# Optimization experiments

Hardware: AMD Instinct MI355X
Metric: run time of the kernel (lower is better)

Reference implementation:

```python
import jax, jax.numpy as jnp
import numpy as np

TEMP = 0.7
ALPHA_ADV = 1.0
BETA_BAND = 0.5
BAND_L = 0.05
BAND_H = 0.2
W_HEUR = 0.5
W_LEAR = 0.5


def setup_inputs() -> dict:
    key = jax.random.key(0)
    ks = jax.random.split(key, 6)
    B, Sn, C, H, W = 2, 5, 64, 192, 192
    hid = 64
    return {
        "S": jax.random.normal(ks[0], (B, C, H, W), jnp.float32),
        "T": jax.random.normal(ks[1], (B, Sn, C, H, W), jnp.float32),
        "adapt_w": jax.random.normal(ks[2], (Sn, C, C), jnp.float32) / np.sqrt(C).astype(np.float32),
        "adapt_b": jnp.zeros((Sn, C), jnp.float32),
        "r_w1": jax.random.normal(ks[3], (hid, Sn * C * 3), jnp.float32) * 0.05,
        "r_b1": jnp.zeros((hid,), jnp.float32),
        "r_w2": jax.random.normal(ks[4], (Sn, hid), jnp.float32) * 0.05,
        "r_b2": jnp.zeros((Sn,), jnp.float32),
        "ema_mu": jnp.zeros((1, Sn, C, 1, 1), jnp.float32),
        "ema_sigma": jnp.ones((1, Sn, C, 1, 1), jnp.float32),
        "ema_proxy": jnp.zeros((1, Sn, 1, 1, 1), jnp.float32),
    }


def reference(S, T, adapt_w, adapt_b, r_w1, r_b1, r_w2, r_b2, ema_mu, ema_sigma, ema_proxy):
    B, Sn, C, H, W = T.shape
    bias = adapt_b[None, :, :, None, None]
    # per-sweep 1x1 conv == per-sweep channel matmul
    T_adapt = jnp.einsum('sdc,bschw->bsdhw', adapt_w, T) + bias          # [B,S,C,H,W]
    S_rep = jnp.einsum('sdc,bchw->bsdhw', adapt_w, S) + bias             # [B,S,C,H,W]
    Tz = (T_adapt - ema_mu) / ema_sigma
    Sz = (S_rep - ema_mu) / ema_sigma
    delta = Tz - Sz
    proxy = jnp.mean(delta * delta, axis=2, keepdims=True)               # [B,S,1,H,W]
    cur = jnp.mean(proxy, axis=(0, 3, 4), keepdims=True)                 # [1,S,1,1,1]
    # heuristic score (gamma_ucb = 0 -> no UCB term)
    impr = jax.lax.stop_gradient(ema_proxy - cur)
    adv = impr - jnp.mean(impr, axis=1, keepdims=True)
    below = jnp.maximum(BAND_L - cur, 0.0)
    above = jnp.maximum(cur - BAND_H, 0.0)
    band = -(below * below + above * above)
    score = ALPHA_ADV * adv + BETA_BAND * band                           # [1,S,1,1,1]
    score_heur = jnp.broadcast_to(score, proxy.shape)[:, :, 0]           # [B,S,H,W]
    # learned router: concat along channel of each sweep then 1x1 MLP
    x = jnp.concatenate([Sz, Tz, delta], axis=2).reshape(B, Sn * 3 * C, H, W)
    h = jax.nn.relu(jnp.einsum('oi,bihw->bohw', r_w1, x) + r_b1[None, :, None, None])
    score_learn = jnp.einsum('oi,bihw->bohw', r_w2, h) + r_b2[None, :, None, None]
    logits = W_HEUR * score_heur + W_LEAR * score_learn                  # [B,S,H,W]
    weights = jax.nn.softmax(logits / TEMP, axis=1)                      # soft gating over sweeps
    return weights
```

## Files before the change

kernel.cpp:

```cpp
#include <hip/hip_runtime.h>
#include <math.h>

#define HWSZ 36864
#define NWID 2304

typedef short bf16x8 __attribute__((ext_vector_type(8)));
typedef float f32x16 __attribute__((ext_vector_type(16)));
typedef unsigned int u32x4 __attribute__((ext_vector_type(4)));

__device__ __forceinline__ unsigned short f2bf(float x) {
    unsigned u = __float_as_uint(x);
    return (unsigned short)((u + 0x7fffu + ((u >> 16) & 1u)) >> 16);
}

__device__ __forceinline__ void block_sync_lds() {
    __builtin_amdgcn_sched_barrier(0);
    asm volatile("s_waitcnt lgkmcnt(0)" ::: "memory");
    __builtin_amdgcn_s_barrier();
    __builtin_amdgcn_sched_barrier(0);
}

__global__ void pre_all(const float* __restrict__ rw1, const float* __restrict__ rb1,
                        const float* __restrict__ aw, const float* __restrict__ ab,
                        const float* __restrict__ mu, const float* __restrict__ sg,
                        unsigned short* __restrict__ AfragW,
                        unsigned short* __restrict__ AfragMS2, float* __restrict__ c1) {
    int i = blockIdx.x * 256 + threadIdx.x;
    if (i < 40960) {
        int s = i / 8192, rem = i % 8192;
        int r = rem / 2048, rem2 = rem % 2048;
        int t = rem2 / 512, q = rem2 % 512;
        int l = q >> 3, e = q & 7;
        int R = 32 * r + (l & 31);
        int k = 16 * t + 8 * (l >> 5) + e;
        float v;
        if (R < 64) {
            v = aw[s * 4096 + R * 64 + k] / sg[s * 64 + R];
        } else {
            int o = R - 64;
            const float* wp = rw1 + o * 960 + s * 192;
            const float* A  = aw + s * 4096 + k;
            const float* G  = sg + s * 64;
            float sum = 0.f;
            #pragma unroll 8
            for (int d = 0; d < 64; ++d)
                sum = fmaf(wp[64 + d] + wp[128 + d], A[d * 64] / G[d], sum);
            v = sum;
        }
        AfragW[i] = f2bf(v);
    } else if (i < 45056) {
        int j = i - 40960;
        int r = j / 2048, rem2 = j % 2048;
        int t = rem2 / 512, q = rem2 % 512;
        int l = q >> 3, e = q & 7;
        int o = 32 * r + (l & 31);
        int k = 16 * t + 8 * (l >> 5) + e;
        float sum = 0.f;
        for (int s = 0; s < 5; ++s) {
            const float* wp = rw1 + o * 960 + s * 192;
            const float* A  = aw + s * 4096 + k;
            const float* G  = sg + s * 64;
            #pragma unroll 8
            for (int d = 0; d < 64; ++d)
                sum = fmaf(wp[d] - wp[128 + d], A[d * 64] / G[d], sum);
        }
        AfragMS2[j] = f2bf(sum);
    } else if (i < 45120) {
        int o = i - 45056;
        float sum = rb1[o];
        for (int s = 0; s < 5; ++s) {
            const float* wp = rw1 + o * 960 + s * 192;
            #pragma unroll 8
            for (int d = 0; d < 64; ++d) {
                int sd = s * 64 + d;
                sum = fmaf(wp[d] + wp[64 + d], (ab[sd] - mu[sd]) / sg[sd], sum);
            }
        }
        c1[o] = sum;
    }
}

__global__ __launch_bounds__(128, 4) void fused_main(
        const float* __restrict__ S, const float* __restrict__ T,
        const unsigned short* __restrict__ AfragW, const unsigned short* __restrict__ AfragMS2,
        const float* __restrict__ c1, const float* __restrict__ rw2, const float* __restrict__ rb2,
        float* __restrict__ slearn, float* __restrict__ partial) {
    __shared__ __align__(16) unsigned short sTile[2048];
    __shared__ __align__(16) unsigned short tbuf[2][2048];
    __shared__ float w2s[320];
    __shared__ float c1s[64];
    __shared__ float rb2s[8];
    __shared__ float wred[5][2];
    __shared__ float hpart[2][5][32];

    const int tid = threadIdx.x, lane = tid & 63, w = tid >> 6;
    const int hi = lane >> 5, pxm = lane & 31;
    const int blk = blockIdx.x;
    const int b = blk / 1152;
    const int pix0 = (blk % 1152) * 32;

    const int o8 = tid >> 4, pq = tid & 15;
    const float* Sp = S + ((size_t)(b * 64 + 8 * o8)) * HWSZ + pix0 + 2 * pq;
    const float* Tp = T + ((size_t)(b * 5 * 64 + 8 * o8)) * HWSZ + pix0 + 2 * pq;

    float2 RS[8], R[8];
    #pragma unroll
    for (int j = 0; j < 8; ++j) RS[j] = *(const float2*)(Sp + (size_t)j * HWSZ);
    #pragma unroll
    for (int j = 0; j < 8; ++j) R[j] = *(const float2*)(Tp + (size_t)j * HWSZ);

    for (int i = tid; i < 320; i += 128) w2s[i] = rw2[i];
    if (tid < 64) c1s[tid] = c1[tid];
    if (tid < 5)  rb2s[tid] = rb2[tid];

    auto slot = [](int px) { return px ^ (px >> 3); };

    auto packWrite = [&](unsigned short* dst, const float2* Rv) {
        #pragma unroll
        for (int pi = 0; pi < 2; ++pi) {
            int px = 2 * pq + pi;
            u32x4 v;
            #pragma unroll
            for (int jj = 0; jj < 4; ++jj) {
                float a = pi ? Rv[2 * jj].y : Rv[2 * jj].x;
                float c = pi ? Rv[2 * jj + 1].y : Rv[2 * jj + 1].x;
                v[jj] = (unsigned)f2bf(a) | ((unsigned)f2bf(c) << 16);
            }
            *(u32x4*)&dst[(o8 * 32 + slot(px)) * 8] = v;
        }
    };
    auto loadT = [&](float2* Rv, int s) {
        const float* p = Tp + (size_t)(s * 64) * HWSZ;
        #pragma unroll
        for (int j = 0; j < 8; ++j) Rv[j] = *(const float2*)(p + (size_t)j * HWSZ);
    };
    auto ldsB = [&](const unsigned short* buf, int kt) -> bf16x8 {
        return *(const bf16x8*)&buf[((kt * 2 + hi) * 32 + slot(pxm)) * 8];
    };

    const bf16x8* am = (const bf16x8*)AfragMS2 + lane;
    bf16x8 msf[4];
    #pragma unroll
    for (int kt = 0; kt < 4; ++kt) msf[kt] = am[(w * 4 + kt) * 64];

    packWrite(sTile, RS);
    block_sync_lds();

    bf16x8 bS[4];
    #pragma unroll
    for (int kt = 0; kt < 4; ++kt) bS[kt] = ldsB(sTile, kt);

    f32x16 hacc;
    #pragma unroll
    for (int i = 0; i < 16; ++i) hacc[i] = 0.f;
    #pragma unroll
    for (int kt = 0; kt < 4; ++kt)
        hacc = __builtin_amdgcn_mfma_f32_32x32x16_bf16(msf[kt], bS[kt], hacc, 0, 0, 0);

    packWrite(tbuf[0], R);
    loadT(R, 1);
    block_sync_lds();

    const bf16x8* afw = (const bf16x8*)AfragW + lane;

    #pragma unroll
    for (int s = 0; s < 5; ++s) {
        const unsigned short* cur = tbuf[s & 1];
        unsigned short* nxt = tbuf[(s + 1) & 1];

        bf16x8 fD[4], fM[4];
        #pragma unroll
        for (int kt = 0; kt < 4; ++kt) fD[kt] = afw[((s * 4 + w) * 4 + kt) * 64];
        #pragma unroll
        for (int kt = 0; kt < 4; ++kt) fM[kt] = afw[((s * 4 + 2 + w) * 4 + kt) * 64];

        if (s < 4) {
            packWrite(nxt, R);
            if (s < 3) loadT(R, s + 2);
        }

        f32x16 dacc;
        #pragma unroll
        for (int i = 0; i < 16; ++i) dacc[i] = 0.f;
        #pragma unroll
        for (int kt = 0; kt < 4; ++kt)
            dacc = __builtin_amdgcn_mfma_f32_32x32x16_bf16(fD[kt], bS[kt], dacc, 0, 0, 0);
        #pragma unroll
        for (int i = 0; i < 16; ++i) dacc[i] = -dacc[i];
        #pragma unroll
        for (int kt = 0; kt < 4; ++kt) {
            bf16x8 bT = ldsB(cur, kt);
            dacc = __builtin_amdgcn_mfma_f32_32x32x16_bf16(fD[kt], bT, dacc, 0, 0, 0);
            hacc = __builtin_amdgcn_mfma_f32_32x32x16_bf16(fM[kt], bT, hacc, 0, 0, 0);
        }

        float sq = 0.f;
        #pragma unroll
        for (int i = 0; i < 16; ++i) sq = fmaf(dacc[i], dacc[i], sq);
        #pragma unroll
        for (int m = 1; m < 64; m <<= 1) sq += __shfl_xor(sq, m, 64);
        if (lane == 0) wred[s][w] = sq;

        block_sync_lds();
    }

    #pragma unroll
    for (int i = 0; i < 16; ++i) {
        int row = (i & 3) + 8 * (i >> 2) + 4 * hi + 32 * w;
        hacc[i] = fmaxf(hacc[i] + c1s[row], 0.f);
    }
    #pragma unroll
    for (int sp = 0; sp < 5; ++sp) {
        float d = 0.f;
        #pragma unroll
        for (int i = 0; i < 16; ++i) {
            int row = (i & 3) + 8 * (i >> 2) + 4 * hi + 32 * w;
            d = fmaf(w2s[sp * 64 + row], hacc[i], d);
        }
        d += __shfl_xor(d, 32, 64);
        if (hi == 0) hpart[w][sp][pxm] = d;
    }
    block_sync_lds();
    if (tid < 5) partial[blk * 5 + tid] = wred[tid][0] + wred[tid][1];
    for (int i = tid; i < 160; i += 128) {
        int sp = i >> 5, px = i & 31;
        slearn[((size_t)(b * 5 + sp)) * HWSZ + pix0 + px] =
            hpart[0][sp][px] + hpart[1][sp][px] + rb2s[sp];
    }
}

__global__ void score_kernel(const float* __restrict__ partial,
                             const float* __restrict__ ema_proxy,
                             float* __restrict__ scoreBuf) {
    __shared__ float red[256];
    __shared__ float cur[5];
    int tid = threadIdx.x;
    for (int s = 0; s < 5; ++s) {
        float sum = 0.f;
        for (int i = tid; i < NWID; i += 256) sum += partial[i * 5 + s];
        red[tid] = sum;
        __syncthreads();
        for (int off = 128; off > 0; off >>= 1) {
            if (tid < off) red[tid] += red[tid + off];
            __syncthreads();
        }
        if (tid == 0) cur[s] = red[0] * (1.0f / (64.0f * 2.0f * HWSZ));
        __syncthreads();
    }
    if (tid == 0) {
        float impr[5]; float m = 0.f;
        for (int s = 0; s < 5; ++s) { impr[s] = ema_proxy[s] - cur[s]; m += impr[s]; }
        m *= 0.2f;
        for (int s = 0; s < 5; ++s) {
            float adv = impr[s] - m;
            float c = cur[s];
            float below = fmaxf(0.05f - c, 0.f);
            float above = fmaxf(c - 0.2f, 0.f);
            float band = -(below * below + above * above);
            scoreBuf[s] = 1.0f * adv + 0.5f * band;
        }
    }
}

__global__ void softmax_kernel(const float* __restrict__ slearn,
                               const float* __restrict__ scoreBuf,
                               float* __restrict__ out) {
    int i = blockIdx.x * 256 + threadIdx.x;
    if (i >= 2 * HWSZ) return;
    int b = i / HWSZ, p = i % HWSZ;
    float l[5];
    float mx = -1e30f;
    #pragma unroll
    for (int s = 0; s < 5; ++s) {
        float v = (0.5f * scoreBuf[s] + 0.5f * slearn[((size_t)(b * 5 + s)) * HWSZ + p]) / 0.7f;
        l[s] = v;
        mx = fmaxf(mx, v);
    }
    float sum = 0.f;
    #pragma unroll
    for (int s = 0; s < 5; ++s) { l[s] = expf(l[s] - mx); sum += l[s]; }
    float inv = 1.0f / sum;
    #pragma unroll
    for (int s = 0; s < 5; ++s) out[((size_t)(b * 5 + s)) * HWSZ + p] = l[s] * inv;
}

extern "C" void kernel_launch(void* const* d_in, const int* in_sizes, int n_in,
                              void* d_out, int out_size, void* d_ws, size_t ws_size,
                              hipStream_t stream) {
    const float* S   = (const float*)d_in[0];
    const float* T   = (const float*)d_in[1];
    const float* aw  = (const float*)d_in[2];
    const float* ab  = (const float*)d_in[3];
    const float* rw1 = (const float*)d_in[4];
    const float* rb1 = (const float*)d_in[5];
    const float* rw2 = (const float*)d_in[6];
    const float* rb2 = (const float*)d_in[7];
    const float* mu  = (const float*)d_in[8];
    const float* sg  = (const float*)d_in[9];
    const float* ep  = (const float*)d_in[10];

    float* ws = (float*)d_ws;
    float* c1f      = ws;
    float* scoreBuf = ws + 64;
    float* partial  = ws + 72;
    unsigned short* AfragW   = (unsigned short*)(ws + 11592);
    unsigned short* AfragMS2 = (unsigned short*)(ws + 32072);
    float* slearn   = ws + 34120;
    float* out = (float*)d_out;

    pre_all<<<177, 256, 0, stream>>>(rw1, rb1, aw, ab, mu, sg, AfragW, AfragMS2, c1f);
    fused_main<<<NWID, 128, 0, stream>>>(S, T, AfragW, AfragMS2, c1f, rw2, rb2, slearn, partial);
    score_kernel<<<1, 256, 0, stream>>>(partial, ep, scoreBuf);
    softmax_kernel<<<288, 256, 0, stream>>>(slearn, scoreBuf, out);
}
```

Baseline: 66.04 us.

## Process two 32-pixel tiles per block and double-buffer weight fragments

Each block now handles 64 pixels as two independent 32-pixel sub-tiles, so the grid is halved and the per-sweep weight fragments loaded from global memory are reused across both tiles. Weight fragments for the next sweep are prefetched into a second register set while the current sweep computes. Register and LDS use roughly doubles, so launch bounds drop to 2 blocks per SM-equivalent, trading occupancy for more loads in flight per wave and more MFMA work per fragment load.

```diff
diff --git a/kernel.cpp b/kernel.cpp
--- a/kernel.cpp
+++ b/kernel.cpp
@@ -3,6 +3,7 @@
 
 #define HWSZ 36864
 #define NWID 2304
+#define NBLK6 1152
 
 typedef short bf16x8 __attribute__((ext_vector_type(8)));
 typedef float f32x16 __attribute__((ext_vector_type(16)));
@@ -80,34 +81,40 @@
     }
 }
 
-__global__ __launch_bounds__(128, 4) void fused_main(
+__global__ __launch_bounds__(128, 2) void fused_main(
         const float* __restrict__ S, const float* __restrict__ T,
         const unsigned short* __restrict__ AfragW, const unsigned short* __restrict__ AfragMS2,
         const float* __restrict__ c1, const float* __restrict__ rw2, const float* __restrict__ rb2,
         float* __restrict__ slearn, float* __restrict__ partial) {
-    __shared__ __align__(16) unsigned short sTile[2048];
-    __shared__ __align__(16) unsigned short tbuf[2][2048];
+    __shared__ __align__(16) unsigned short sTileA[2048], sTileB[2048];
+    __shared__ __align__(16) unsigned short tbufA[2][2048], tbufB[2][2048];
     __shared__ float w2s[320];
     __shared__ float c1s[64];
     __shared__ float rb2s[8];
-    __shared__ float wred[5][2];
-    __shared__ float hpart[2][5][32];
+    __shared__ float wredA[5][2], wredB[5][2];
+    __shared__ float hpartA[2][5][32], hpartB[2][5][32];
 
     const int tid = threadIdx.x, lane = tid & 63, w = tid >> 6;
     const int hi = lane >> 5, pxm = lane & 31;
     const int blk = blockIdx.x;
-    const int b = blk / 1152;
-    const int pix0 = (blk % 1152) * 32;
+    const int b = blk / 576;
+    const int pix0 = (blk % 576) * 64;
 
     const int o8 = tid >> 4, pq = tid & 15;
-    const float* Sp = S + ((size_t)(b * 64 + 8 * o8)) * HWSZ + pix0 + 2 * pq;
-    const float* Tp = T + ((size_t)(b * 5 * 64 + 8 * o8)) * HWSZ + pix0 + 2 * pq;
-
-    float2 RS[8], R[8];
-    #pragma unroll
-    for (int j = 0; j < 8; ++j) RS[j] = *(const float2*)(Sp + (size_t)j * HWSZ);
-    #pragma unroll
-    for (int j = 0; j < 8; ++j) R[j] = *(const float2*)(Tp + (size_t)j * HWSZ);
+    const float* SpA = S + ((size_t)(b * 64 + 8 * o8)) * HWSZ + pix0 + 2 * pq;
+    const float* TpA = T + ((size_t)(b * 5 * 64 + 8 * o8)) * HWSZ + pix0 + 2 * pq;
+    const float* SpB = SpA + 32;
+    const float* TpB = TpA + 32;
+
+    float2 RSA[8], RSB[8], RA[8], RB[8];
+    #pragma unroll
+    for (int j = 0; j < 8; ++j) RSA[j] = *(const float2*)(SpA + (size_t)j * HWSZ);
+    #pragma unroll
+    for (int j = 0; j < 8; ++j) RSB[j] = *(const float2*)(SpB + (size_t)j * HWSZ);
+    #pragma unroll
+    for (int j = 0; j < 8; ++j) RA[j] = *(const float2*)(TpA + (size_t)j * HWSZ);
+    #pragma unroll
+    for (int j = 0; j < 8; ++j) RB[j] = *(const float2*)(TpB + (size_t)j * HWSZ);
 
     for (int i = tid; i < 320; i += 128) w2s[i] = rw2[i];
     if (tid < 64) c1s[tid] = c1[tid];
@@ -129,8 +136,8 @@
             *(u32x4*)&dst[(o8 * 32 + slot(px)) * 8] = v;
         }
     };
-    auto loadT = [&](float2* Rv, int s) {
-        const float* p = Tp + (size_t)(s * 64) * HWSZ;
+    auto loadT = [&](float2* Rv, const float* Tp_, int s) {
+        const float* p = Tp_ + (size_t)(s * 64) * HWSZ;
         #pragma unroll
         for (int j = 0; j < 8; ++j) Rv[j] = *(const float2*)(p + (size_t)j * HWSZ);
     };
@@ -143,89 +150,135 @@
     #pragma unroll
     for (int kt = 0; kt < 4; ++kt) msf[kt] = am[(w * 4 + kt) * 64];
 
-    packWrite(sTile, RS);
+    const bf16x8* afw = (const bf16x8*)AfragW + lane;
+    bf16x8 fD0[4], fM0[4], fD1[4], fM1[4];
+    #pragma unroll
+    for (int kt = 0; kt < 4; ++kt) fD0[kt] = afw[((0 * 4 + w) * 4 + kt) * 64];
+    #pragma unroll
+    for (int kt = 0; kt < 4; ++kt) fM0[kt] = afw[((0 * 4 + 2 + w) * 4 + kt) * 64];
+
+    packWrite(sTileA, RSA);
+    packWrite(sTileB, RSB);
     block_sync_lds();
 
-    bf16x8 bS[4];
-    #pragma unroll
-    for (int kt = 0; kt < 4; ++kt) bS[kt] = ldsB(sTile, kt);
-
-    f32x16 hacc;
-    #pragma unroll
-    for (int i = 0; i < 16; ++i) hacc[i] = 0.f;
-    #pragma unroll
-    for (int kt = 0; kt < 4; ++kt)
-        hacc = __builtin_amdgcn_mfma_f32_32x32x16_bf16(msf[kt], bS[kt], hacc, 0, 0, 0);
-
-    packWrite(tbuf[0], R);
-    loadT(R, 1);
+    bf16x8 bSA[4], bSB[4];
+    #pragma unroll
+    for (int kt = 0; kt < 4; ++kt) { bSA[kt] = ldsB(sTileA, kt); bSB[kt] = ldsB(sTileB, kt); }
+
+    f32x16 hA, hB;
+    #pragma unroll
+    for (int i = 0; i < 16; ++i) { hA[i] = 0.f; hB[i] = 0.f; }
+    #pragma unroll
+    for (int kt = 0; kt < 4; ++kt) {
+        hA = __builtin_amdgcn_mfma_f32_32x32x16_bf16(msf[kt], bSA[kt], hA, 0, 0, 0);
+        hB = __builtin_amdgcn_mfma_f32_32x32x16_bf16(msf[kt], bSB[kt], hB, 0, 0, 0);
+    }
+
+    packWrite(tbufA[0], RA);
+    packWrite(tbufB[0], RB);
+    loadT(RA, TpA, 1);
+    loadT(RB, TpB, 1);
     block_sync_lds();
 
-    const bf16x8* afw = (const bf16x8*)AfragW + lane;
-
     #pragma unroll
     for (int s = 0; s < 5; ++s) {
-        const unsigned short* cur = tbuf[s & 1];
-        unsigned short* nxt = tbuf[(s + 1) & 1];
-
-        bf16x8 fD[4], fM[4];
-        #pragma unroll
-        for (int kt = 0; kt < 4; ++kt) fD[kt] = afw[((s * 4 + w) * 4 + kt) * 64];
-        #pragma unroll
-        for (int kt = 0; kt < 4; ++kt) fM[kt] = afw[((s * 4 + 2 + w) * 4 + kt) * 64];
+        const unsigned short* curA = tbufA[s & 1];
+        unsigned short* nxtA       = tbufA[(s + 1) & 1];
+        const unsigned short* curB = tbufB[s & 1];
+        unsigned short* nxtB       = tbufB[(s + 1) & 1];
+        const bf16x8* fDc = (s & 1) ? fD1 : fD0;
+        const bf16x8* fMc = (s & 1) ? fM1 : fM0;
+        bf16x8* fDn = (s & 1) ? fD0 : fD1;
+        bf16x8* fMn = (s & 1) ? fM0 : fM1;
 
         if (s < 4) {
-            packWrite(nxt, R);
-            if (s < 3) loadT(R, s + 2);
-        }
-
-        f32x16 dacc;
-        #pragma unroll
-        for (int i = 0; i < 16; ++i) dacc[i] = 0.f;
-        #pragma unroll
-        for (int kt = 0; kt < 4; ++kt)
-            dacc = __builtin_amdgcn_mfma_f32_32x32x16_bf16(fD[kt], bS[kt], dacc, 0, 0, 0);
-        #pragma unroll
-        for (int i = 0; i < 16; ++i) dacc[i] = -dacc[i];
-        #pragma unroll
-        for (int kt = 0; kt < 4; ++kt) {
-            bf16x8 bT = ldsB(cur, kt);
-            dacc = __builtin_amdgcn_mfma_f32_32x32x16_bf16(fD[kt], bT, dacc, 0, 0, 0);
-            hacc = __builtin_amdgcn_mfma_f32_32x32x16_bf16(fM[kt], bT, hacc, 0, 0, 0);
-        }
-
-        float sq = 0.f;
-        #pragma unroll
-        for (int i = 0; i < 16; ++i) sq = fmaf(dacc[i], dacc[i], sq);
-        #pragma unroll
-        for (int m = 1; m < 64; m <<= 1) sq += __shfl_xor(sq, m, 64);
-        if (lane == 0) wred[s][w] = sq;
-
+            #pragma unroll
+            for (int kt = 0; kt < 4; ++kt) fDn[kt] = afw[(((s + 1) * 4 + w) * 4 + kt) * 64];
+            #pragma unroll
+            for (int kt = 0; kt < 4; ++kt) fMn[kt] = afw[(((s + 1) * 4 + 2 + w) * 4 + kt) * 64];
+            packWrite(nxtA, RA);
+            packWrite(nxtB, RB);
+            if (s < 3) { loadT(RA, TpA, s + 2); loadT(RB, TpB, s + 2); }
+        }
+
+        {
+            f32x16 dacc;
+            #pragma unroll
+            for (int i = 0; i < 16; ++i) dacc[i] = 0.f;
+            #pragma unroll
+            for (int kt = 0; kt < 4; ++kt)
+                dacc = __builtin_amdgcn_mfma_f32_32x32x16_bf16(fDc[kt], bSA[kt], dacc, 0, 0, 0);
+            #pragma unroll
+            for (int i = 0; i < 16; ++i) dacc[i] = -dacc[i];
+            #pragma unroll
+            for (int kt = 0; kt < 4; ++kt) {
+                bf16x8 bT = ldsB(curA, kt);
+                dacc = __builtin_amdgcn_mfma_f32_32x32x16_bf16(fDc[kt], bT, dacc, 0, 0, 0);
+                hA   = __builtin_amdgcn_mfma_f32_32x32x16_bf16(fMc[kt], bT, hA, 0, 0, 0);
+            }
+            float sq = 0.f;
+            #pragma unroll
+            for (int i = 0; i < 16; ++i) sq = fmaf(dacc[i], dacc[i], sq);
+            #pragma unroll
+            for (int m = 1; m < 64; m <<= 1) sq += __shfl_xor(sq, m, 64);
+            if (lane == 0) wredA[s][w] = sq;
+        }
+        {
+            f32x16 dacc;
+            #pragma unroll
+            for (int i = 0; i < 16; ++i) dacc[i] = 0.f;
+            #pragma unroll
+            for (int kt = 0; kt < 4; ++kt)
+                dacc = __builtin_amdgcn_mfma_f32_32x32x16_bf16(fDc[kt], bSB[kt], dacc, 0, 0, 0);
+            #pragma unroll
+            for (int i = 0; i < 16; ++i) dacc[i] = -dacc[i];
+            #pragma unroll
+            for (int kt = 0; kt < 4; ++kt) {
+                bf16x8 bT = ldsB(curB, kt);
+                dacc = __builtin_amdgcn_mfma_f32_32x32x16_bf16(fDc[kt], bT, dacc, 0, 0, 0);
+                hB   = __builtin_amdgcn_mfma_f32_32x32x16_bf16(fMc[kt], bT, hB, 0, 0, 0);
+            }
+            float sq = 0.f;
+            #pragma unroll
+            for (int i = 0; i < 16; ++i) sq = fmaf(dacc[i], dacc[i], sq);
+            #pragma unroll
+            for (int m = 1; m < 64; m <<= 1) sq += __shfl_xor(sq, m, 64);
+            if (lane == 0) wredB[s][w] = sq;
+        }
         block_sync_lds();
     }
 
     #pragma unroll
     for (int i = 0; i < 16; ++i) {
         int row = (i & 3) + 8 * (i >> 2) + 4 * hi + 32 * w;
-        hacc[i] = fmaxf(hacc[i] + c1s[row], 0.f);
+        hA[i] = fmaxf(hA[i] + c1s[row], 0.f);
+        hB[i] = fmaxf(hB[i] + c1s[row], 0.f);
     }
     #pragma unroll
     for (int sp = 0; sp < 5; ++sp) {
-        float d = 0.f;
+        float dA = 0.f, dB = 0.f;
         #pragma unroll
         for (int i = 0; i < 16; ++i) {
             int row = (i & 3) + 8 * (i >> 2) + 4 * hi + 32 * w;
-            d = fmaf(w2s[sp * 64 + row], hacc[i], d);
-        }
-        d += __shfl_xor(d, 32, 64);
-        if (hi == 0) hpart[w][sp][pxm] = d;
+            dA = fmaf(w2s[sp * 64 + row], hA[i], dA);
+            dB = fmaf(w2s[sp * 64 + row], hB[i], dB);
+        }
+        dA += __shfl_xor(dA, 32, 64);
+        dB += __shfl_xor(dB, 32, 64);
+        if (hi == 0) { hpartA[w][sp][pxm] = dA; hpartB[w][sp][pxm] = dB; }
     }
     block_sync_lds();
-    if (tid < 5) partial[blk * 5 + tid] = wred[tid][0] + wred[tid][1];
-    for (int i = tid; i < 160; i += 128) {
-        int sp = i >> 5, px = i & 31;
-        slearn[((size_t)(b * 5 + sp)) * HWSZ + pix0 + px] =
-            hpart[0][sp][px] + hpart[1][sp][px] + rb2s[sp];
+    if (tid < 5) {
+        partial[(blk * 2 + 0) * 5 + tid] = wredA[tid][0] + wredA[tid][1];
+    } else if (tid < 10) {
+        int t5 = tid - 5;
+        partial[(blk * 2 + 1) * 5 + t5] = wredB[t5][0] + wredB[t5][1];
+    }
+    for (int i = tid; i < 320; i += 128) {
+        int sp = i >> 6, px = i & 63;
+        float v = (px < 32) ? (hpartA[0][sp][px] + hpartA[1][sp][px])
+                            : (hpartB[0][sp][px - 32] + hpartB[1][sp][px - 32]);
+        slearn[((size_t)(b * 5 + sp)) * HWSZ + pix0 + px] = v + rb2s[sp];
     }
 }
 
@@ -309,7 +362,7 @@
     float* out = (float*)d_out;
 
     pre_all<<<177, 256, 0, stream>>>(rw1, rb1, aw, ab, mu, sg, AfragW, AfragMS2, c1f);
-    fused_main<<<NWID, 128, 0, stream>>>(S, T, AfragW, AfragMS2, c1f, rw2, rb2, slearn, partial);
+    fused_main<<<NBLK6, 128, 0, stream>>>(S, T, AfragW, AfragMS2, c1f, rw2, rb2, slearn, partial);
     score_kernel<<<1, 256, 0, stream>>>(partial, ep, scoreBuf);
     softmax_kernel<<<288, 256, 0, stream>>>(slearn, scoreBuf, out);
 }
```

Result: faster. 63.51 us (-3.8%).
